# Performance work log

Hardware: AMD Instinct MI355X
Metric: run time of the kernel (lower is better)

## Reference

```python
import jax, jax.numpy as jnp
import numpy as np


def _mlp(x, W1, b1, W2, b2):
    # x: [..., 3d]; Linear weights stored torch-style: W1 [d, 3d], W2 [1, d]
    h = jax.nn.relu(jnp.einsum('...i,di->...d', x, W1) + b1)
    return jax.nn.sigmoid(jnp.einsum('...d,od->...o', h, W2) + b2)[..., 0]


def setup_inputs() -> dict:
    key = jax.random.key(0)
    ks = jax.random.split(key, 6)
    N, d, E, K = 1000000, 64, 65536, 16
    embeds = jax.random.normal(ks[0], (N, d), dtype=jnp.float32)
    pos = jax.random.randint(ks[1], (E, 2), 0, N, dtype=jnp.int64)
    neg = jax.random.randint(ks[2], (E, K, 2), 0, N, dtype=jnp.int64)
    # xavier-uniform init as in the torch module
    lim1 = float(np.sqrt(6.0 / (3 * d + d)))
    lim2 = float(np.sqrt(6.0 / (d + 1)))
    W1 = jax.random.uniform(ks[3], (d, 3 * d), jnp.float32, -lim1, lim1)
    b1 = jnp.zeros((d,), jnp.float32)
    W2 = jax.random.uniform(ks[4], (1, d), jnp.float32, -lim2, lim2)
    b2 = jnp.zeros((1,), jnp.float32)
    return {"embeds": embeds, "pos": pos, "neg": neg,
            "W1": W1, "b1": b1, "W2": W2, "b2": b2}


def reference(embeds, pos, neg, W1, b1, W2, b2):
    # positive pairs: [E, 3d]
    pu = embeds[pos[:, 0]]
    pv = embeds[pos[:, 1]]
    pos_emb = jnp.concatenate([pu, pv, pu * pv], axis=-1)
    # negative pairs: [E, K, 3d]
    nu = embeds[neg[:, :, 0]]
    nv = embeds[neg[:, :, 1]]
    neg_emb = jnp.concatenate([nu, nv, nu * nv], axis=-1)
    pos_scr = jnp.exp(_mlp(pos_emb, W1, b1, W2, b2))          # [E]
    neg_scr = jnp.exp(_mlp(neg_emb, W1, b1, W2, b2))          # [E, K]
    denom = jnp.sum(neg_scr, axis=-1) + pos_scr               # [E]
    loss = -jnp.sum(pos_scr / (denom + 1e-8) + 1e-8)
    return loss
```

## Files before the change

kernel.cpp:

```cpp
#include <hip/hip_runtime.h>
#include <math.h>

#define N_EMB   1000000
#define D       64
#define E_PAIRS 65536
#define K_NEG   16
#define P_TOTAL (E_PAIRS * (K_NEG + 1))
#define PPB     128

typedef __attribute__((ext_vector_type(8))) short  short8;
typedef __attribute__((ext_vector_type(4))) float  float4v;

static __device__ __forceinline__ unsigned short f2bf(float f) {
    unsigned int x = __float_as_uint(f);
    unsigned int r = (x + 0x7fffu + ((x >> 16) & 1u)) >> 16;
    return (unsigned short)r;
}

static __device__ __forceinline__ short8 pack8(float4 a, float4 b) {
    short8 r;
    r[0] = (short)f2bf(a.x); r[1] = (short)f2bf(a.y);
    r[2] = (short)f2bf(a.z); r[3] = (short)f2bf(a.w);
    r[4] = (short)f2bf(b.x); r[5] = (short)f2bf(b.y);
    r[6] = (short)f2bf(b.z); r[7] = (short)f2bf(b.w);
    return r;
}

static __device__ __forceinline__ float4 mul4(float4 a, float4 b) {
    return make_float4(a.x * b.x, a.y * b.y, a.z * b.z, a.w * b.w);
}

static __device__ __forceinline__ void load_frags(const float* __restrict__ embeds,
                                                  int ui, int vi, int quad,
                                                  short8* fr)
{
    const float* up = embeds + (long long)ui * D + quad * 8;
    const float* vp = embeds + (long long)vi * D + quad * 8;
    float4 ua = *(const float4*)(up);
    float4 ub = *(const float4*)(up + 4);
    float4 uc = *(const float4*)(up + 32);
    float4 ud = *(const float4*)(up + 36);
    float4 va = *(const float4*)(vp);
    float4 vb = *(const float4*)(vp + 4);
    float4 vc = *(const float4*)(vp + 32);
    float4 vd = *(const float4*)(vp + 36);
    fr[0] = pack8(ua, ub);
    fr[1] = pack8(uc, ud);
    fr[2] = pack8(va, vb);
    fr[3] = pack8(vc, vd);
    fr[4] = pack8(mul4(ua, va), mul4(ub, vb));
    fr[5] = pack8(mul4(uc, vc), mul4(ud, vd));
}

__global__ __launch_bounds__(256)
void prep_kernel(const float* __restrict__ W1, unsigned short* __restrict__ W1bf)
{
    int i = blockIdx.x * 256 + threadIdx.x;
    if (i < 64 * 192) W1bf[i] = f2bf(W1[i]);
}

__global__ __launch_bounds__(256, 4)
void score_kernel(const float* __restrict__ embeds,
                  const int*   __restrict__ pos,
                  const int*   __restrict__ neg,
                  const unsigned short* __restrict__ W1bf,
                  const float* __restrict__ b1,
                  const float* __restrict__ W2,
                  const float* __restrict__ b2,
                  float*       __restrict__ scores)
{
    const int t    = threadIdx.x;
    const int lane = t & 63;
    const int wave = t >> 6;
    const int c16  = lane & 15;
    const int quad = lane >> 4;
    const int pw   = blockIdx.x * PPB + wave * 32;

    const int p0 = pw + c16;
    const int p1 = pw + 16 + c16;
    int2 i0, i1;
    if (pw < E_PAIRS) {
        i0 = ((const int2*)pos)[p0];
        i1 = ((const int2*)pos)[p1];
    } else {
        i0 = ((const int2*)neg)[p0 - E_PAIRS];
        i1 = ((const int2*)neg)[p1 - E_PAIRS];
    }

    short8 a0[6], a1[6];
    load_frags(embeds, i0.x, i0.y, quad, a0);
    load_frags(embeds, i1.x, i1.y, quad, a1);

    float4v acc[2][4];
    #pragma unroll
    for (int mt = 0; mt < 2; ++mt)
        #pragma unroll
        for (int nt = 0; nt < 4; ++nt)
            acc[mt][nt] = (float4v){0.f, 0.f, 0.f, 0.f};

    #pragma unroll
    for (int ks = 0; ks < 6; ++ks) {
        const int koff = ks * 32 + quad * 8;
        short8 bfrag[4];
        #pragma unroll
        for (int nt = 0; nt < 4; ++nt)
            bfrag[nt] = *(const short8*)(W1bf + (nt * 16 + c16) * 192 + koff);
        #pragma unroll
        for (int nt = 0; nt < 4; ++nt) {
            acc[0][nt] = __builtin_amdgcn_mfma_f32_16x16x32_bf16(a0[ks], bfrag[nt], acc[0][nt], 0, 0, 0);
            acc[1][nt] = __builtin_amdgcn_mfma_f32_16x16x32_bf16(a1[ks], bfrag[nt], acc[1][nt], 0, 0, 0);
        }
    }

    float b1v[4], w2v[4];
    #pragma unroll
    for (int nt = 0; nt < 4; ++nt) {
        b1v[nt] = b1[nt * 16 + c16];
        w2v[nt] = W2[nt * 16 + c16];
    }
    const float b2v = b2[0];

    #pragma unroll
    for (int mt = 0; mt < 2; ++mt) {
        #pragma unroll
        for (int reg = 0; reg < 4; ++reg) {
            float s = 0.f;
            #pragma unroll
            for (int nt = 0; nt < 4; ++nt) {
                float h = acc[mt][nt][reg] + b1v[nt];
                s += (h > 0.f ? h : 0.f) * w2v[nt];
            }
            s += __shfl_xor(s, 1);
            s += __shfl_xor(s, 2);
            s += __shfl_xor(s, 4);
            s += __shfl_xor(s, 8);
            if (c16 == 0) {
                float sig = 1.f / (1.f + expf(-(s + b2v)));
                scores[pw + mt * 16 + quad * 4 + reg] = expf(sig);
            }
        }
    }
}

__global__ __launch_bounds__(256)
void reduce_kernel(const float* __restrict__ scores, float* __restrict__ partials)
{
    __shared__ float sdata[256];
    int e = blockIdx.x * 256 + threadIdx.x;
    float pos_s = scores[e];
    const float* ns = scores + E_PAIRS + (size_t)e * K_NEG;
    float nsum = 0.f;
    #pragma unroll
    for (int c = 0; c < 4; ++c) {
        float4 v = *(const float4*)(ns + c * 4);
        nsum += v.x + v.y + v.z + v.w;
    }
    float term = pos_s / (pos_s + nsum + 1e-8f) + 1e-8f;
    sdata[threadIdx.x] = term;
    __syncthreads();
    for (int s = 128; s > 0; s >>= 1) {
        if (threadIdx.x < s) sdata[threadIdx.x] += sdata[threadIdx.x + s];
        __syncthreads();
    }
    if (threadIdx.x == 0) partials[blockIdx.x] = sdata[0];
}

__global__ __launch_bounds__(256)
void final_kernel(const float* __restrict__ partials, float* __restrict__ out)
{
    __shared__ float sdata[256];
    sdata[threadIdx.x] = partials[threadIdx.x];
    __syncthreads();
    for (int s = 128; s > 0; s >>= 1) {
        if (threadIdx.x < s) sdata[threadIdx.x] += sdata[threadIdx.x + s];
        __syncthreads();
    }
    if (threadIdx.x == 0) out[0] = -sdata[0];
}

extern "C" void kernel_launch(void* const* d_in, const int* in_sizes, int n_in,
                              void* d_out, int out_size, void* d_ws, size_t ws_size,
                              hipStream_t stream)
{
    const float* embeds = (const float*)d_in[0];
    const int*   pos    = (const int*)d_in[1];
    const int*   neg    = (const int*)d_in[2];
    const float* W1     = (const float*)d_in[3];
    const float* b1     = (const float*)d_in[4];
    const float* W2     = (const float*)d_in[5];
    const float* b2     = (const float*)d_in[6];
    float* out = (float*)d_out;

    float* scores   = (float*)d_ws;
    float* partials = scores + P_TOTAL;
    unsigned short* W1bf = (unsigned short*)(partials + 256);

    prep_kernel<<<48, 256, 0, stream>>>(W1, W1bf);
    score_kernel<<<P_TOTAL / PPB, 256, 0, stream>>>(embeds, pos, neg, W1bf, b1, W2, b2, scores);
    reduce_kernel<<<E_PAIRS / 256, 256, 0, stream>>>(scores, partials);
    final_kernel<<<1, 256, 0, stream>>>(partials, out);
}
```

Before: 469.8 us.

## Pre-convert embedding table to fp16 to halve gather bytes, use f16 MFMA

Adds a prep kernel that converts the whole fp32 embedding table and W1 to fp16 in workspace on every call. The score kernel then gathers 128-byte fp16 rows instead of 256-byte fp32 rows, computes the u*v product with packed half multiplies, and uses f16 MFMA. The aim is to cut random-gather traffic and conversion ALU work, and to let the half-size table fit better in the last-level cache. The cost is a full streaming read and write of the table each call. The two-stage final reduction becomes an atomicAdd after a memset, and a bf16 fallback path is kept for when the workspace is too small.

```diff
diff --git a/kernel.cpp b/kernel.cpp
--- a/kernel.cpp
+++ b/kernel.cpp
@@ -1,4 +1,5 @@
 #include <hip/hip_runtime.h>
+#include <hip/hip_fp16.h>
 #include <math.h>
 
 #define N_EMB   1000000
@@ -8,8 +9,10 @@
 #define P_TOTAL (E_PAIRS * (K_NEG + 1))
 #define PPB     128
 
-typedef __attribute__((ext_vector_type(8))) short  short8;
-typedef __attribute__((ext_vector_type(4))) float  float4v;
+typedef __attribute__((ext_vector_type(8))) short     short8;
+typedef __attribute__((ext_vector_type(8))) _Float16  half8;
+typedef __attribute__((ext_vector_type(4))) float     float4v;
+
 
 static __device__ __forceinline__ unsigned short f2bf(float f) {
     unsigned int x = __float_as_uint(f);
@@ -17,57 +20,60 @@
     return (unsigned short)r;
 }
 
-static __device__ __forceinline__ short8 pack8(float4 a, float4 b) {
-    short8 r;
-    r[0] = (short)f2bf(a.x); r[1] = (short)f2bf(a.y);
-    r[2] = (short)f2bf(a.z); r[3] = (short)f2bf(a.w);
-    r[4] = (short)f2bf(b.x); r[5] = (short)f2bf(b.y);
-    r[6] = (short)f2bf(b.z); r[7] = (short)f2bf(b.w);
-    return r;
-}
-
-static __device__ __forceinline__ float4 mul4(float4 a, float4 b) {
-    return make_float4(a.x * b.x, a.y * b.y, a.z * b.z, a.w * b.w);
-}
-
-static __device__ __forceinline__ void load_frags(const float* __restrict__ embeds,
-                                                  int ui, int vi, int quad,
-                                                  short8* fr)
-{
-    const float* up = embeds + (long long)ui * D + quad * 8;
-    const float* vp = embeds + (long long)vi * D + quad * 8;
-    float4 ua = *(const float4*)(up);
-    float4 ub = *(const float4*)(up + 4);
-    float4 uc = *(const float4*)(up + 32);
-    float4 ud = *(const float4*)(up + 36);
-    float4 va = *(const float4*)(vp);
-    float4 vb = *(const float4*)(vp + 4);
-    float4 vc = *(const float4*)(vp + 32);
-    float4 vd = *(const float4*)(vp + 36);
-    fr[0] = pack8(ua, ub);
-    fr[1] = pack8(uc, ud);
-    fr[2] = pack8(va, vb);
-    fr[3] = pack8(vc, vd);
-    fr[4] = pack8(mul4(ua, va), mul4(ub, vb));
-    fr[5] = pack8(mul4(uc, vc), mul4(ud, vd));
-}
+static __device__ __forceinline__ unsigned int h2mul(unsigned int a, unsigned int b) {
+    union { unsigned int u; __half2 h; } A, B, R;
+    A.u = a; B.u = b;
+    R.h = __hmul2(A.h, B.h);
+    return R.u;
+}
+
+static __device__ __forceinline__ uint4 h2mul4(uint4 a, uint4 b) {
+    return make_uint4(h2mul(a.x, b.x), h2mul(a.y, b.y),
+                      h2mul(a.z, b.z), h2mul(a.w, b.w));
+}
+
+static __device__ __forceinline__ float4v mfma16f(uint4 a, uint4 b, float4v c) {
+    union { uint4 u; half8 h; } A, B;
+    A.u = a; B.u = b;
+    return __builtin_amdgcn_mfma_f32_16x16x32_f16(A.h, B.h, c, 0, 0, 0);
+}
+
 
 __global__ __launch_bounds__(256)
-void prep_kernel(const float* __restrict__ W1, unsigned short* __restrict__ W1bf)
-{
-    int i = blockIdx.x * 256 + threadIdx.x;
-    if (i < 64 * 192) W1bf[i] = f2bf(W1[i]);
+void prep_f16(const float* __restrict__ embeds, const float* __restrict__ W1,
+              __half* __restrict__ emb16, __half* __restrict__ W1h)
+{
+    const int nchunks = N_EMB * D / 8;
+    const int stride  = gridDim.x * blockDim.x;
+    for (int c = blockIdx.x * blockDim.x + threadIdx.x; c < nchunks; c += stride) {
+        const float* src = embeds + (size_t)c * 8;
+        float4 f0 = *(const float4*)(src);
+        float4 f1 = *(const float4*)(src + 4);
+        union { unsigned short s[8]; uint4 u; } o;
+        o.s[0] = __half_as_ushort(__float2half(f0.x));
+        o.s[1] = __half_as_ushort(__float2half(f0.y));
+        o.s[2] = __half_as_ushort(__float2half(f0.z));
+        o.s[3] = __half_as_ushort(__float2half(f0.w));
+        o.s[4] = __half_as_ushort(__float2half(f1.x));
+        o.s[5] = __half_as_ushort(__float2half(f1.y));
+        o.s[6] = __half_as_ushort(__float2half(f1.z));
+        o.s[7] = __half_as_ushort(__float2half(f1.w));
+        *((uint4*)emb16 + c) = o.u;
+    }
+    if (blockIdx.x == 0)
+        for (int i = threadIdx.x; i < 64 * 192; i += 256)
+            W1h[i] = __float2half(W1[i]);
 }
 
 __global__ __launch_bounds__(256, 4)
-void score_kernel(const float* __restrict__ embeds,
-                  const int*   __restrict__ pos,
-                  const int*   __restrict__ neg,
-                  const unsigned short* __restrict__ W1bf,
-                  const float* __restrict__ b1,
-                  const float* __restrict__ W2,
-                  const float* __restrict__ b2,
-                  float*       __restrict__ scores)
+void score_f16(const __half* __restrict__ emb,
+               const int*    __restrict__ pos,
+               const int*    __restrict__ neg,
+               const __half* __restrict__ W1h,
+               const float*  __restrict__ b1,
+               const float*  __restrict__ W2,
+               const float*  __restrict__ b2,
+               float*        __restrict__ scores)
 {
     const int t    = threadIdx.x;
     const int lane = t & 63;
@@ -87,9 +93,24 @@
         i1 = ((const int2*)neg)[p1 - E_PAIRS];
     }
 
-    short8 a0[6], a1[6];
-    load_frags(embeds, i0.x, i0.y, quad, a0);
-    load_frags(embeds, i1.x, i1.y, quad, a1);
+    const __half* u0p = emb + (long long)i0.x * D + quad * 8;
+    const __half* v0p = emb + (long long)i0.y * D + quad * 8;
+    const __half* u1p = emb + (long long)i1.x * D + quad * 8;
+    const __half* v1p = emb + (long long)i1.y * D + quad * 8;
+
+    uint4 a0[6], a1[6];
+    a0[0] = *(const uint4*)(u0p);
+    a0[1] = *(const uint4*)(u0p + 32);
+    a0[2] = *(const uint4*)(v0p);
+    a0[3] = *(const uint4*)(v0p + 32);
+    a1[0] = *(const uint4*)(u1p);
+    a1[1] = *(const uint4*)(u1p + 32);
+    a1[2] = *(const uint4*)(v1p);
+    a1[3] = *(const uint4*)(v1p + 32);
+    a0[4] = h2mul4(a0[0], a0[2]);
+    a0[5] = h2mul4(a0[1], a0[3]);
+    a1[4] = h2mul4(a1[0], a1[2]);
+    a1[5] = h2mul4(a1[1], a1[3]);
 
     float4v acc[2][4];
     #pragma unroll
@@ -101,14 +122,14 @@
     #pragma unroll
     for (int ks = 0; ks < 6; ++ks) {
         const int koff = ks * 32 + quad * 8;
-        short8 bfrag[4];
+        uint4 bfrag[4];
         #pragma unroll
         for (int nt = 0; nt < 4; ++nt)
-            bfrag[nt] = *(const short8*)(W1bf + (nt * 16 + c16) * 192 + koff);
+            bfrag[nt] = *(const uint4*)(W1h + (nt * 16 + c16) * 192 + koff);
         #pragma unroll
         for (int nt = 0; nt < 4; ++nt) {
-            acc[0][nt] = __builtin_amdgcn_mfma_f32_16x16x32_bf16(a0[ks], bfrag[nt], acc[0][nt], 0, 0, 0);
-            acc[1][nt] = __builtin_amdgcn_mfma_f32_16x16x32_bf16(a1[ks], bfrag[nt], acc[1][nt], 0, 0, 0);
+            acc[0][nt] = mfma16f(a0[ks], bfrag[nt], acc[0][nt]);
+            acc[1][nt] = mfma16f(a1[ks], bfrag[nt], acc[1][nt]);
         }
     }
 
@@ -142,8 +163,130 @@
     }
 }
 
+
+static __device__ __forceinline__ short8 pack8(float4 a, float4 b) {
+    short8 r;
+    r[0] = (short)f2bf(a.x); r[1] = (short)f2bf(a.y);
+    r[2] = (short)f2bf(a.z); r[3] = (short)f2bf(a.w);
+    r[4] = (short)f2bf(b.x); r[5] = (short)f2bf(b.y);
+    r[6] = (short)f2bf(b.z); r[7] = (short)f2bf(b.w);
+    return r;
+}
+static __device__ __forceinline__ float4 mul4(float4 a, float4 b) {
+    return make_float4(a.x * b.x, a.y * b.y, a.z * b.z, a.w * b.w);
+}
+static __device__ __forceinline__ void load_frags(const float* __restrict__ embeds,
+                                                  int ui, int vi, int quad, short8* fr)
+{
+    const float* up = embeds + (long long)ui * D + quad * 8;
+    const float* vp = embeds + (long long)vi * D + quad * 8;
+    float4 ua = *(const float4*)(up);
+    float4 ub = *(const float4*)(up + 4);
+    float4 uc = *(const float4*)(up + 32);
+    float4 ud = *(const float4*)(up + 36);
+    float4 va = *(const float4*)(vp);
+    float4 vb = *(const float4*)(vp + 4);
+    float4 vc = *(const float4*)(vp + 32);
+    float4 vd = *(const float4*)(vp + 36);
+    fr[0] = pack8(ua, ub); fr[1] = pack8(uc, ud);
+    fr[2] = pack8(va, vb); fr[3] = pack8(vc, vd);
+    fr[4] = pack8(mul4(ua, va), mul4(ub, vb));
+    fr[5] = pack8(mul4(uc, vc), mul4(ud, vd));
+}
+
 __global__ __launch_bounds__(256)
-void reduce_kernel(const float* __restrict__ scores, float* __restrict__ partials)
+void prep_w1bf(const float* __restrict__ W1, unsigned short* __restrict__ W1bf)
+{
+    int i = blockIdx.x * 256 + threadIdx.x;
+    if (i < 64 * 192) W1bf[i] = f2bf(W1[i]);
+}
+
+__global__ __launch_bounds__(256, 4)
+void score_f32(const float* __restrict__ embeds,
+               const int*   __restrict__ pos,
+               const int*   __restrict__ neg,
+               const unsigned short* __restrict__ W1bf,
+               const float* __restrict__ b1,
+               const float* __restrict__ W2,
+               const float* __restrict__ b2,
+               float*       __restrict__ scores)
+{
+    const int t    = threadIdx.x;
+    const int lane = t & 63;
+    const int wave = t >> 6;
+    const int c16  = lane & 15;
+    const int quad = lane >> 4;
+    const int pw   = blockIdx.x * PPB + wave * 32;
+
+    const int p0 = pw + c16;
+    const int p1 = pw + 16 + c16;
+    int2 i0, i1;
+    if (pw < E_PAIRS) {
+        i0 = ((const int2*)pos)[p0];
+        i1 = ((const int2*)pos)[p1];
+    } else {
+        i0 = ((const int2*)neg)[p0 - E_PAIRS];
+        i1 = ((const int2*)neg)[p1 - E_PAIRS];
+    }
+
+    short8 a0[6], a1[6];
+    load_frags(embeds, i0.x, i0.y, quad, a0);
+    load_frags(embeds, i1.x, i1.y, quad, a1);
+
+    float4v acc[2][4];
+    #pragma unroll
+    for (int mt = 0; mt < 2; ++mt)
+        #pragma unroll
+        for (int nt = 0; nt < 4; ++nt)
+            acc[mt][nt] = (float4v){0.f, 0.f, 0.f, 0.f};
+
+    #pragma unroll
+    for (int ks = 0; ks < 6; ++ks) {
+        const int koff = ks * 32 + quad * 8;
+        short8 bfrag[4];
+        #pragma unroll
+        for (int nt = 0; nt < 4; ++nt)
+            bfrag[nt] = *(const short8*)(W1bf + (nt * 16 + c16) * 192 + koff);
+        #pragma unroll
+        for (int nt = 0; nt < 4; ++nt) {
+            acc[0][nt] = __builtin_amdgcn_mfma_f32_16x16x32_bf16(a0[ks], bfrag[nt], acc[0][nt], 0, 0, 0);
+            acc[1][nt] = __builtin_amdgcn_mfma_f32_16x16x32_bf16(a1[ks], bfrag[nt], acc[1][nt], 0, 0, 0);
+        }
+    }
+
+    float b1v[4], w2v[4];
+    #pragma unroll
+    for (int nt = 0; nt < 4; ++nt) {
+        b1v[nt] = b1[nt * 16 + c16];
+        w2v[nt] = W2[nt * 16 + c16];
+    }
+    const float b2v = b2[0];
+
+    #pragma unroll
+    for (int mt = 0; mt < 2; ++mt) {
+        #pragma unroll
+        for (int reg = 0; reg < 4; ++reg) {
+            float s = 0.f;
+            #pragma unroll
+            for (int nt = 0; nt < 4; ++nt) {
+                float h = acc[mt][nt][reg] + b1v[nt];
+                s += (h > 0.f ? h : 0.f) * w2v[nt];
+            }
+            s += __shfl_xor(s, 1);
+            s += __shfl_xor(s, 2);
+            s += __shfl_xor(s, 4);
+            s += __shfl_xor(s, 8);
+            if (c16 == 0) {
+                float sig = 1.f / (1.f + expf(-(s + b2v)));
+                scores[pw + mt * 16 + quad * 4 + reg] = expf(sig);
+            }
+        }
+    }
+}
+
+
+__global__ __launch_bounds__(256)
+void reduce_atomic(const float* __restrict__ scores, float* __restrict__ out)
 {
     __shared__ float sdata[256];
     int e = blockIdx.x * 256 + threadIdx.x;
@@ -162,21 +305,9 @@
         if (threadIdx.x < s) sdata[threadIdx.x] += sdata[threadIdx.x + s];
         __syncthreads();
     }
-    if (threadIdx.x == 0) partials[blockIdx.x] = sdata[0];
-}
-
-__global__ __launch_bounds__(256)
-void final_kernel(const float* __restrict__ partials, float* __restrict__ out)
-{
-    __shared__ float sdata[256];
-    sdata[threadIdx.x] = partials[threadIdx.x];
-    __syncthreads();
-    for (int s = 128; s > 0; s >>= 1) {
-        if (threadIdx.x < s) sdata[threadIdx.x] += sdata[threadIdx.x + s];
-        __syncthreads();
-    }
-    if (threadIdx.x == 0) out[0] = -sdata[0];
-}
+    if (threadIdx.x == 0) atomicAdd(out, -sdata[0]);
+}
+
 
 extern "C" void kernel_launch(void* const* d_in, const int* in_sizes, int n_in,
                               void* d_out, int out_size, void* d_ws, size_t ws_size,
@@ -191,12 +322,25 @@
     const float* b2     = (const float*)d_in[6];
     float* out = (float*)d_out;
 
-    float* scores   = (float*)d_ws;
-    float* partials = scores + P_TOTAL;
-    unsigned short* W1bf = (unsigned short*)(partials + 256);
-
-    prep_kernel<<<48, 256, 0, stream>>>(W1, W1bf);
-    score_kernel<<<P_TOTAL / PPB, 256, 0, stream>>>(embeds, pos, neg, W1bf, b1, W2, b2, scores);
-    reduce_kernel<<<E_PAIRS / 256, 256, 0, stream>>>(scores, partials);
-    final_kernel<<<1, 256, 0, stream>>>(partials, out);
-}
+    const size_t EMB16_BYTES = (size_t)N_EMB * D * 2;
+    const size_t need = EMB16_BYTES + (size_t)P_TOTAL * 4 + 64 * 192 * 2;
+
+    hipMemsetAsync(out, 0, sizeof(float), stream);
+
+    if (ws_size >= need) {
+        __half* emb16  = (__half*)d_ws;
+        float*  scores = (float*)((char*)d_ws + EMB16_BYTES);
+        __half* W1h    = (__half*)(scores + P_TOTAL);
+
+        prep_f16<<<2048, 256, 0, stream>>>(embeds, W1, emb16, W1h);
+        score_f16<<<P_TOTAL / PPB, 256, 0, stream>>>(emb16, pos, neg, W1h, b1, W2, b2, scores);
+        reduce_atomic<<<E_PAIRS / 256, 256, 0, stream>>>(scores, out);
+    } else {
+        float* scores = (float*)d_ws;
+        unsigned short* W1bf = (unsigned short*)(scores + P_TOTAL);
+
+        prep_w1bf<<<48, 256, 0, stream>>>(W1, W1bf);
+        score_f32<<<P_TOTAL / PPB, 256, 0, stream>>>(embeds, pos, neg, W1bf, b1, W2, b2, scores);
+        reduce_atomic<<<E_PAIRS / 256, 256, 0, stream>>>(scores, out);
+    }
+}
```

Result: slower. 512.6 us (+9.1%).
